# Kernel tuning notes

Hardware: AMD Instinct MI355X
Metric: run time of the kernel (lower is better)

The kernel has to match this reference:

```python
import jax, jax.numpy as jnp
import numpy as np

HEADS = 16
HEAD_DIM = 64
EMBED = HEADS * HEAD_DIM  # 1024
B, S = 2, 2048


def setup_inputs() -> dict:
    key = jax.random.key(0)
    ks = jax.random.split(key, 9)
    return {
        "value": jax.random.normal(ks[0], (B, S, EMBED), dtype=jnp.float32),
        "key": jax.random.normal(ks[1], (B, S, EMBED), dtype=jnp.float32),
        "query": jax.random.normal(ks[2], (B, S, EMBED), dtype=jnp.float32),
        "mask": jax.random.randint(ks[3], (B, 1, S, S), 0, 2, dtype=jnp.int32),
        "Wq": jax.random.normal(ks[4], (HEAD_DIM, HEAD_DIM), dtype=jnp.float32) * 0.02,
        "Wk": jax.random.normal(ks[5], (HEAD_DIM, HEAD_DIM), dtype=jnp.float32) * 0.02,
        "Wv": jax.random.normal(ks[6], (HEAD_DIM, HEAD_DIM), dtype=jnp.float32) * 0.02,
        "Wo": jax.random.normal(ks[7], (EMBED, EMBED), dtype=jnp.float32) * 0.02,
        "bo": jnp.zeros((EMBED,), dtype=jnp.float32),
    }


def reference(value, key, query, mask, Wq, Wk, Wv, Wo, bo):
    N, Lv = value.shape[0], value.shape[1]
    Lk, Lq = key.shape[1], query.shape[1]
    # Faithful to original: plain reshape (N, heads, len, head_dim), NOT transpose.
    v = value.reshape(N, HEADS, Lv, HEAD_DIM)
    k = key.reshape(N, HEADS, Lk, HEAD_DIM)
    q = query.reshape(N, HEADS, Lq, HEAD_DIM)
    # Per-head Linear (no bias): x @ W.T
    V = jnp.einsum('bhld,ed->bhle', v, Wv)
    K = jnp.einsum('bhld,ed->bhle', k, Wk)
    Q = jnp.einsum('bhld,ed->bhle', q, Wq)
    score = jnp.einsum('bhqd,bhkd->bhqk', Q, K)  # [B,H,Sq,Sk]
    score = jnp.where(mask == 0, jnp.float32(-1e20), score)
    # Faithful quirk: scale by sqrt(embed_size), not sqrt(head_dim)
    scale = jnp.float32(EMBED ** 0.5)
    attn = jax.nn.softmax(score / scale, axis=3)
    out = jnp.einsum('bhqk,bhkd->bhqd', attn, V).reshape(N, Lq, HEADS * HEAD_DIM)
    return out @ Wo.T + bo
```

## Files before the change

### kernel.cpp

```cpp
#include <hip/hip_runtime.h>
#include <hip/hip_bf16.h>
#include <cstdint>
#include <cstddef>

#define S_LEN 2048
#define N_HEADS 16
#define HD 64
#define EMB 1024
#define N_BATCH 2
#define N_BH (N_BATCH * N_HEADS)

typedef __attribute__((ext_vector_type(4))) float f32x4;
typedef __attribute__((ext_vector_type(8))) short bf16x8;
typedef __attribute__((ext_vector_type(4))) short bf16x4;

__device__ __forceinline__ short f2bf(float f) {
    unsigned u = __builtin_bit_cast(unsigned, f);
    unsigned r = (u + 0x7FFFu + ((u >> 16) & 1u)) >> 16;
    return (short)r;
}

__device__ __forceinline__ unsigned packbf(float a, float b) {
    return (unsigned)(unsigned short)f2bf(a) | ((unsigned)(unsigned short)f2bf(b) << 16);
}

__device__ __forceinline__ f32x4 mfma16(bf16x8 a, bf16x8 b, f32x4 c) {
    return __builtin_amdgcn_mfma_f32_16x16x32_bf16(a, b, c, 0, 0, 0);
}

#if __has_builtin(__builtin_amdgcn_exp2f)
__device__ __forceinline__ float fast_exp2(float x) { return __builtin_amdgcn_exp2f(x); }
#else
__device__ __forceinline__ float fast_exp2(float x) { return exp2f(x); }
#endif

__global__ __launch_bounds__(256) void pack_mask_kernel(
    const int* __restrict__ mask, unsigned long long* __restrict__ bits) {
    int wid = (blockIdx.x * 256 + threadIdx.x) >> 6;
    int lane = threadIdx.x & 63;
    const int* src = mask + (size_t)wid * 256 + lane;
    unsigned long long w0 = __ballot(src[0] != 0);
    unsigned long long w1 = __ballot(src[64] != 0);
    unsigned long long w2 = __ballot(src[128] != 0);
    unsigned long long w3 = __ballot(src[192] != 0);
    if (lane == 0) {
        unsigned long long* dst = bits + (size_t)wid * 4;
        dst[0] = w0; dst[1] = w1; dst[2] = w2; dst[3] = w3;
    }
}

__global__ __launch_bounds__(256) void conv_wo_kernel(
    const float* __restrict__ W, short* __restrict__ Wb) {
    int i = blockIdx.x * 256 + threadIdx.x;
    f32x4 v = reinterpret_cast<const f32x4*>(W)[i];
    bf16x4 o = { f2bf(v.x), f2bf(v.y), f2bf(v.z), f2bf(v.w) };
    reinterpret_cast<bf16x4*>(Wb)[i] = o;
}

__global__ __launch_bounds__(256) void proj_kernel(
    const float* __restrict__ q_in, const float* __restrict__ k_in,
    const float* __restrict__ v_in,
    const float* __restrict__ Wq, const float* __restrict__ Wk,
    const float* __restrict__ Wv,
    short* __restrict__ Qb, short* __restrict__ Kb, short* __restrict__ Vt) {
    int rt = blockIdx.x;
    int bh = blockIdx.y;
    int tz = blockIdx.z;
    const float* src = (tz == 0 ? q_in : tz == 1 ? k_in : v_in)
                       + (size_t)bh * S_LEN * HD + (size_t)rt * 64 * HD;
    const float* W = (tz == 0 ? Wq : tz == 1 ? Wk : Wv);

    __shared__ short Al[64 * 72];
    __shared__ short Wl[64 * 72];
    __shared__ short Ol[64 * 72];

    int t = threadIdx.x;
#pragma unroll
    for (int r = 0; r < 4; r++) {
        int f4 = t + 256 * r;
        int row = f4 >> 4;
        int c4 = (f4 & 15) * 4;
        f32x4 a = reinterpret_cast<const f32x4*>(src)[f4];
        bf16x4 ab = { f2bf(a.x), f2bf(a.y), f2bf(a.z), f2bf(a.w) };
        *reinterpret_cast<bf16x4*>(&Al[row * 72 + c4]) = ab;
        f32x4 w = reinterpret_cast<const f32x4*>(W)[f4];
        bf16x4 wb = { f2bf(w.x), f2bf(w.y), f2bf(w.z), f2bf(w.w) };
        *reinterpret_cast<bf16x4*>(&Wl[row * 72 + c4]) = wb;
    }
    __syncthreads();

    int wave = t >> 6, lane = t & 63, quad = lane >> 4, col = lane & 15;
    bf16x8 a0 = *reinterpret_cast<const bf16x8*>(&Al[(wave * 16 + col) * 72 + quad * 8]);
    bf16x8 a1 = *reinterpret_cast<const bf16x8*>(&Al[(wave * 16 + col) * 72 + 32 + quad * 8]);

    const float C1 = 0.04508422002777448f;
    float scl = (tz == 0) ? C1 : 1.0f;

    f32x4 acc[4];
#pragma unroll
    for (int jt = 0; jt < 4; jt++) {
        bf16x8 b0 = *reinterpret_cast<const bf16x8*>(&Wl[(jt * 16 + col) * 72 + quad * 8]);
        bf16x8 b1 = *reinterpret_cast<const bf16x8*>(&Wl[(jt * 16 + col) * 72 + 32 + quad * 8]);
        f32x4 c = {0.f, 0.f, 0.f, 0.f};
        c = mfma16(a0, b0, c);
        c = mfma16(a1, b1, c);
        acc[jt] = c;
    }
    __syncthreads();

    if (tz < 2) {
#pragma unroll
        for (int jt = 0; jt < 4; jt++)
#pragma unroll
            for (int i = 0; i < 4; i++)
                Ol[(wave * 16 + quad * 4 + i) * 72 + jt * 16 + col] = f2bf(acc[jt][i] * scl);
        __syncthreads();
        short* dst = (tz == 0 ? Qb : Kb) + (size_t)bh * S_LEN * HD + (size_t)rt * 64 * HD;
        int row = t >> 2, ck = (t & 3) * 16;
        bf16x8 o0 = *reinterpret_cast<const bf16x8*>(&Ol[row * 72 + ck]);
        bf16x8 o1 = *reinterpret_cast<const bf16x8*>(&Ol[row * 72 + ck + 8]);
        *reinterpret_cast<bf16x8*>(&dst[row * 64 + ck]) = o0;
        *reinterpret_cast<bf16x8*>(&dst[row * 64 + ck + 8]) = o1;
    } else {
#pragma unroll
        for (int jt = 0; jt < 4; jt++)
#pragma unroll
            for (int i = 0; i < 4; i++)
                Ol[(jt * 16 + col) * 72 + wave * 16 + quad * 4 + i] = f2bf(acc[jt][i]);
        __syncthreads();
        short* dst = Vt + (size_t)bh * HD * S_LEN + rt * 64;
        int d = t >> 2, ck = (t & 3) * 16;
        bf16x8 o0 = *reinterpret_cast<const bf16x8*>(&Ol[d * 72 + ck]);
        bf16x8 o1 = *reinterpret_cast<const bf16x8*>(&Ol[d * 72 + ck + 8]);
        *reinterpret_cast<bf16x8*>(&dst[(size_t)d * S_LEN + ck]) = o0;
        *reinterpret_cast<bf16x8*>(&dst[(size_t)d * S_LEN + ck + 8]) = o1;
    }
}

__global__ __launch_bounds__(256, 4) void attn_kernel(
    const short* __restrict__ Qb, const short* __restrict__ Kb,
    const short* __restrict__ Vt, const unsigned long long* __restrict__ mbits,
    short* __restrict__ Xb) {
    int qt = blockIdx.x;
    int bh = blockIdx.y;
    int b = bh >> 4;
    int t = threadIdx.x, wave = t >> 6, lane = t & 63, quad = lane >> 4, col = lane & 15;

    __shared__ short Ks[64 * 64];
    __shared__ short Vs[64 * 64];
    __shared__ short Pl[4][16 * 72];
    short* Pw = &Pl[wave][0];

    const short* Qh = Qb + (size_t)bh * S_LEN * HD;
    const short* Kh = Kb + (size_t)bh * S_LEN * HD;
    const short* Vh = Vt + (size_t)bh * HD * S_LEN;
    int q0w = qt * 64 + wave * 16;
    int q = q0w + col;

    bf16x8 qf0 = *reinterpret_cast<const bf16x8*>(&Qh[(size_t)q * HD + quad * 8]);
    bf16x8 qf1 = *reinterpret_cast<const bf16x8*>(&Qh[(size_t)q * HD + 32 + quad * 8]);
    const unsigned long long* mrow = mbits + (size_t)(b * S_LEN + q) * 32;

    int r0 = t >> 3, r1 = (t + 256) >> 3, cc = t & 7;
    int dst0 = r0 * 64 + ((cc ^ (r0 & 7)) * 8);
    int dst1 = r1 * 64 + ((cc ^ (r1 & 7)) * 8);
    const short* kg0 = Kh + r0 * HD + cc * 8;
    const short* kg1 = Kh + r1 * HD + cc * 8;
    const short* vg0 = Vh + (size_t)r0 * S_LEN + cc * 8;
    const short* vg1 = Vh + (size_t)r1 * S_LEN + cc * 8;

    bf16x8 pk0 = *reinterpret_cast<const bf16x8*>(kg0);
    bf16x8 pk1 = *reinterpret_cast<const bf16x8*>(kg1);
    bf16x8 pv0 = *reinterpret_cast<const bf16x8*>(vg0);
    bf16x8 pv1 = *reinterpret_cast<const bf16x8*>(vg1);
    *reinterpret_cast<bf16x8*>(&Ks[dst0]) = pk0;
    *reinterpret_cast<bf16x8*>(&Ks[dst1]) = pk1;
    *reinterpret_cast<bf16x8*>(&Vs[dst0]) = pv0;
    *reinterpret_cast<bf16x8*>(&Vs[dst1]) = pv1;
    __syncthreads();

    unsigned bs[4];
#pragma unroll
    for (int i = 0; i < 4; i++) bs[i] = 1u << (quad * 4 + i);
    const short one_bf = (short)0x3F80;
    bf16x8 ones = { one_bf, one_bf, one_bf, one_bf, one_bf, one_bf, one_bf, one_bf };

    int sw = quad ^ (col & 7);
    unsigned long long mw = mrow[0];

    f32x4 o[4];
    f32x4 l = {0.f, 0.f, 0.f, 0.f};
#pragma unroll
    for (int dt = 0; dt < 4; dt++) o[dt] = (f32x4){0.f, 0.f, 0.f, 0.f};

    for (int kt = 0; kt < 32; kt++) {
        unsigned long long mw_n;
        if (kt < 31) {
            pk0 = *reinterpret_cast<const bf16x8*>(kg0 + (kt + 1) * 4096);
            pk1 = *reinterpret_cast<const bf16x8*>(kg1 + (kt + 1) * 4096);
            pv0 = *reinterpret_cast<const bf16x8*>(vg0 + (kt + 1) * 64);
            pv1 = *reinterpret_cast<const bf16x8*>(vg1 + (kt + 1) * 64);
            mw_n = mrow[kt + 1];
        }
        f32x4 s[4];
#pragma unroll
        for (int mt = 0; mt < 4; mt++) {
            const short* kbase = &Ks[(mt * 16 + col) * 64];
            bf16x8 ka0 = *reinterpret_cast<const bf16x8*>(&kbase[sw * 8]);
            bf16x8 ka1 = *reinterpret_cast<const bf16x8*>(&kbase[(sw ^ 4) * 8]);
            f32x4 c = {0.f, 0.f, 0.f, 0.f};
            c = mfma16(ka0, qf0, c);
            c = mfma16(ka1, qf1, c);
            s[mt] = c;
        }
#pragma unroll
        for (int mt = 0; mt < 4; mt++) {
            unsigned g = (unsigned)(mw >> (mt * 16));
            float p0 = fast_exp2((g & bs[0]) ? s[mt][0] : -200.0f);
            float p1 = fast_exp2((g & bs[1]) ? s[mt][1] : -200.0f);
            float p2 = fast_exp2((g & bs[2]) ? s[mt][2] : -200.0f);
            float p3 = fast_exp2((g & bs[3]) ? s[mt][3] : -200.0f);
            uint2 dw = { packbf(p0, p1), packbf(p2, p3) };
            *reinterpret_cast<uint2*>(&Pw[col * 72 + mt * 16 + quad * 4]) = dw;
        }
#pragma unroll
        for (int c = 0; c < 2; c++) {
            bf16x8 pb = *reinterpret_cast<const bf16x8*>(&Pw[col * 72 + c * 32 + quad * 8]);
            l = mfma16(ones, pb, l);
#pragma unroll
            for (int dt = 0; dt < 4; dt++) {
                bf16x8 va = *reinterpret_cast<const bf16x8*>(
                    &Vs[(dt * 16 + col) * 64 + (((c * 4 + quad) ^ (col & 7)) * 8)]);
                o[dt] = mfma16(va, pb, o[dt]);
            }
        }
        __syncthreads();
        if (kt < 31) {
            *reinterpret_cast<bf16x8*>(&Ks[dst0]) = pk0;
            *reinterpret_cast<bf16x8*>(&Ks[dst1]) = pk1;
            *reinterpret_cast<bf16x8*>(&Vs[dst0]) = pv0;
            *reinterpret_cast<bf16x8*>(&Vs[dst1]) = pv1;
            mw = mw_n;
            __syncthreads();
        }
    }

    float inv = 1.0f / l[0];
#pragma unroll
    for (int dt = 0; dt < 4; dt++) {
        uint2 dw = { packbf(o[dt][0] * inv, o[dt][1] * inv),
                     packbf(o[dt][2] * inv, o[dt][3] * inv) };
        *reinterpret_cast<uint2*>(&Pw[col * 72 + dt * 16 + quad * 4]) = dw;
    }
    int rr = lane >> 2, ck = (lane & 3) * 16;
    bf16x8 x0 = *reinterpret_cast<const bf16x8*>(&Pw[rr * 72 + ck]);
    bf16x8 x1 = *reinterpret_cast<const bf16x8*>(&Pw[rr * 72 + ck + 8]);
    short* Xrow = Xb + (size_t)bh * S_LEN * HD + (size_t)(q0w + rr) * HD;
    *reinterpret_cast<bf16x8*>(&Xrow[ck]) = x0;
    *reinterpret_cast<bf16x8*>(&Xrow[ck + 8]) = x1;
}

__global__ __launch_bounds__(256, 4) void final_kernel(
    const short* __restrict__ Xb, const short* __restrict__ Wob,
    const float* __restrict__ bo, float* __restrict__ out) {
    int nb = blockIdx.x;
    int mb = blockIdx.y;
    int t = threadIdx.x, wave = t >> 6, lane = t & 63, quad = lane >> 4, col = lane & 15;
    __shared__ short Xs[64 * 64];
    __shared__ short Ws[64 * 64];
    __shared__ float Olds[64 * 68];

    int m0 = mb * 64, n0 = nb * 64;
    int r0 = t >> 3, r1 = (t + 256) >> 3, cc = t & 7;
    int dst0 = r0 * 64 + ((cc ^ (r0 & 7)) * 8);
    int dst1 = r1 * 64 + ((cc ^ (r1 & 7)) * 8);
    const short* xg0 = Xb + (size_t)(m0 + r0) * EMB + cc * 8;
    const short* xg1 = Xb + (size_t)(m0 + r1) * EMB + cc * 8;
    const short* wg0 = Wob + (size_t)(n0 + r0) * EMB + cc * 8;
    const short* wg1 = Wob + (size_t)(n0 + r1) * EMB + cc * 8;

    bf16x8 px0 = *reinterpret_cast<const bf16x8*>(xg0);
    bf16x8 px1 = *reinterpret_cast<const bf16x8*>(xg1);
    bf16x8 pw0 = *reinterpret_cast<const bf16x8*>(wg0);
    bf16x8 pw1 = *reinterpret_cast<const bf16x8*>(wg1);
    *reinterpret_cast<bf16x8*>(&Xs[dst0]) = px0;
    *reinterpret_cast<bf16x8*>(&Xs[dst1]) = px1;
    *reinterpret_cast<bf16x8*>(&Ws[dst0]) = pw0;
    *reinterpret_cast<bf16x8*>(&Ws[dst1]) = pw1;
    __syncthreads();

    int sw = quad ^ (col & 7);
    f32x4 acc[4];
#pragma unroll
    for (int jt = 0; jt < 4; jt++) acc[jt] = (f32x4){0.f, 0.f, 0.f, 0.f};

    for (int s = 0; s < 16; s++) {
        if (s < 15) {
            px0 = *reinterpret_cast<const bf16x8*>(xg0 + (s + 1) * 64);
            px1 = *reinterpret_cast<const bf16x8*>(xg1 + (s + 1) * 64);
            pw0 = *reinterpret_cast<const bf16x8*>(wg0 + (s + 1) * 64);
            pw1 = *reinterpret_cast<const bf16x8*>(wg1 + (s + 1) * 64);
        }
        const short* arow = &Xs[(wave * 16 + col) * 64];
        bf16x8 a0 = *reinterpret_cast<const bf16x8*>(&arow[sw * 8]);
        bf16x8 a1 = *reinterpret_cast<const bf16x8*>(&arow[(sw ^ 4) * 8]);
#pragma unroll
        for (int jt = 0; jt < 4; jt++) {
            const short* brow = &Ws[(jt * 16 + col) * 64];
            bf16x8 b0 = *reinterpret_cast<const bf16x8*>(&brow[sw * 8]);
            bf16x8 b1 = *reinterpret_cast<const bf16x8*>(&brow[(sw ^ 4) * 8]);
            acc[jt] = mfma16(a0, b0, acc[jt]);
            acc[jt] = mfma16(a1, b1, acc[jt]);
        }
        __syncthreads();
        if (s < 15) {
            *reinterpret_cast<bf16x8*>(&Xs[dst0]) = px0;
            *reinterpret_cast<bf16x8*>(&Xs[dst1]) = px1;
            *reinterpret_cast<bf16x8*>(&Ws[dst0]) = pw0;
            *reinterpret_cast<bf16x8*>(&Ws[dst1]) = pw1;
            __syncthreads();
        }
    }

#pragma unroll
    for (int jt = 0; jt < 4; jt++)
#pragma unroll
        for (int i = 0; i < 4; i++)
            Olds[(wave * 16 + quad * 4 + i) * 68 + jt * 16 + col] = acc[jt][i];
    __syncthreads();
    int row = t >> 2, ck = (t & 3) * 16;
#pragma unroll
    for (int u = 0; u < 4; u++) {
        f32x4 v = *reinterpret_cast<const f32x4*>(&Olds[row * 68 + ck + u * 4]);
        f32x4 bb = *reinterpret_cast<const f32x4*>(&bo[n0 + ck + u * 4]);
        v.x += bb.x; v.y += bb.y; v.z += bb.z; v.w += bb.w;
        *reinterpret_cast<f32x4*>(&out[(size_t)(m0 + row) * EMB + n0 + ck + u * 4]) = v;
    }
}

extern "C" void kernel_launch(void* const* d_in, const int* in_sizes, int n_in,
                              void* d_out, int out_size, void* d_ws, size_t ws_size,
                              hipStream_t stream) {
    const float* value = (const float*)d_in[0];
    const float* key_  = (const float*)d_in[1];
    const float* query = (const float*)d_in[2];
    const int*   mask  = (const int*)d_in[3];
    const float* Wq = (const float*)d_in[4];
    const float* Wk = (const float*)d_in[5];
    const float* Wv = (const float*)d_in[6];
    const float* Wo = (const float*)d_in[7];
    const float* bo = (const float*)d_in[8];
    float* out = (float*)d_out;

    char* ws = (char*)d_ws;
    short* Qb  = (short*)(ws);
    short* Kb  = (short*)(ws + (size_t)8  * 1048576);
    short* Vt  = (short*)(ws + (size_t)16 * 1048576);
    short* Xb  = (short*)(ws + (size_t)24 * 1048576);
    short* Wob = (short*)(ws + (size_t)32 * 1048576);
    unsigned long long* mbits =
        (unsigned long long*)(ws + (size_t)34 * 1048576);

    pack_mask_kernel<<<dim3((N_BATCH * S_LEN * S_LEN) / 1024), dim3(256), 0, stream>>>(mask, mbits);
    conv_wo_kernel<<<dim3((EMB * EMB) / (256 * 4)), dim3(256), 0, stream>>>(Wo, Wob);
    proj_kernel<<<dim3(S_LEN / 64, N_BH, 3), dim3(256), 0, stream>>>(
        query, key_, value, Wq, Wk, Wv, Qb, Kb, Vt);
    attn_kernel<<<dim3(S_LEN / 64, N_BH), dim3(256), 0, stream>>>(Qb, Kb, Vt, mbits, Xb);
    final_kernel<<<dim3(EMB / 64, (N_BATCH * S_LEN) / 64), dim3(256), 0, stream>>>(
        Xb, Wob, bo, out);
}
```

Before: 217.6 us.

## Switch to fp16 MFMA, merge prep kernels, use 128-query attention blocks

Merges mask packing, Wo conversion and the Q/K/V projections into one prep launch, removing two kernel launches. Replaces bf16 with fp16 throughout, using packed round-toward-zero conversion and fp16 MFMA, which cuts the conversion instruction count. Attention blocks now use 512 threads covering 128 queries, so each K/V tile staged in shared memory serves twice as many queries and each thread loads half as much. fp16 range is a risk for unnormalized values, but the inputs here appear scaled small.

```diff
diff --git a/kernel.cpp b/kernel.cpp
--- a/kernel.cpp
+++ b/kernel.cpp
@@ -11,21 +11,16 @@
 #define N_BH (N_BATCH * N_HEADS)
 
 typedef __attribute__((ext_vector_type(4))) float f32x4;
-typedef __attribute__((ext_vector_type(8))) short bf16x8;
-typedef __attribute__((ext_vector_type(4))) short bf16x4;
-
-__device__ __forceinline__ short f2bf(float f) {
-    unsigned u = __builtin_bit_cast(unsigned, f);
-    unsigned r = (u + 0x7FFFu + ((u >> 16) & 1u)) >> 16;
-    return (short)r;
-}
-
-__device__ __forceinline__ unsigned packbf(float a, float b) {
-    return (unsigned)(unsigned short)f2bf(a) | ((unsigned)(unsigned short)f2bf(b) << 16);
-}
-
-__device__ __forceinline__ f32x4 mfma16(bf16x8 a, bf16x8 b, f32x4 c) {
-    return __builtin_amdgcn_mfma_f32_16x16x32_bf16(a, b, c, 0, 0, 0);
+typedef __attribute__((ext_vector_type(8))) short short8;
+typedef __attribute__((ext_vector_type(8))) _Float16 half8;
+typedef __attribute__((ext_vector_type(2))) _Float16 half2v;
+
+__device__ __forceinline__ f32x4 mfma16h(half8 a, half8 b, f32x4 c) {
+    return __builtin_amdgcn_mfma_f32_16x16x32_f16(a, b, c, 0, 0, 0);
+}
+
+__device__ __forceinline__ unsigned pkh(float a, float b) {
+    return __builtin_bit_cast(unsigned, __builtin_amdgcn_cvt_pkrtz(a, b));
 }
 
 #if __has_builtin(__builtin_amdgcn_exp2f)
@@ -34,64 +29,67 @@
 __device__ __forceinline__ float fast_exp2(float x) { return exp2f(x); }
 #endif
 
-__global__ __launch_bounds__(256) void pack_mask_kernel(
-    const int* __restrict__ mask, unsigned long long* __restrict__ bits) {
-    int wid = (blockIdx.x * 256 + threadIdx.x) >> 6;
-    int lane = threadIdx.x & 63;
-    const int* src = mask + (size_t)wid * 256 + lane;
-    unsigned long long w0 = __ballot(src[0] != 0);
-    unsigned long long w1 = __ballot(src[64] != 0);
-    unsigned long long w2 = __ballot(src[128] != 0);
-    unsigned long long w3 = __ballot(src[192] != 0);
-    if (lane == 0) {
-        unsigned long long* dst = bits + (size_t)wid * 4;
-        dst[0] = w0; dst[1] = w1; dst[2] = w2; dst[3] = w3;
-    }
-}
-
-__global__ __launch_bounds__(256) void conv_wo_kernel(
-    const float* __restrict__ W, short* __restrict__ Wb) {
-    int i = blockIdx.x * 256 + threadIdx.x;
-    f32x4 v = reinterpret_cast<const f32x4*>(W)[i];
-    bf16x4 o = { f2bf(v.x), f2bf(v.y), f2bf(v.z), f2bf(v.w) };
-    reinterpret_cast<bf16x4*>(Wb)[i] = o;
-}
-
-__global__ __launch_bounds__(256) void proj_kernel(
+__global__ __launch_bounds__(256) void prep_kernel(
     const float* __restrict__ q_in, const float* __restrict__ k_in,
     const float* __restrict__ v_in,
     const float* __restrict__ Wq, const float* __restrict__ Wk,
-    const float* __restrict__ Wv,
-    short* __restrict__ Qb, short* __restrict__ Kb, short* __restrict__ Vt) {
-    int rt = blockIdx.x;
-    int bh = blockIdx.y;
-    int tz = blockIdx.z;
+    const float* __restrict__ Wv, const float* __restrict__ Wo,
+    const int* __restrict__ mask,
+    short* __restrict__ Qb, short* __restrict__ Kb, short* __restrict__ Vt,
+    short* __restrict__ Woh, unsigned long long* __restrict__ bits) {
+    __shared__ short Al[64 * 72];
+    __shared__ short Wl[64 * 72];
+    __shared__ short Ol[64 * 72];
+    int bx = blockIdx.x;
+    int t = threadIdx.x;
+
+    if (bx >= 3072) {
+        if (bx < 11264) {
+            int wid = ((bx - 3072) * 256 + t) >> 6;
+            int lane = t & 63;
+            const int* src = mask + (size_t)wid * 256 + lane;
+            unsigned long long w0 = __ballot(src[0] != 0);
+            unsigned long long w1 = __ballot(src[64] != 0);
+            unsigned long long w2 = __ballot(src[128] != 0);
+            unsigned long long w3 = __ballot(src[192] != 0);
+            if (lane == 0) {
+                unsigned long long* dst = bits + (size_t)wid * 4;
+                dst[0] = w0; dst[1] = w1; dst[2] = w2; dst[3] = w3;
+            }
+        } else {
+            int i = (bx - 11264) * 256 + t;
+            f32x4 a = reinterpret_cast<const f32x4*>(Wo)[i * 2];
+            f32x4 b = reinterpret_cast<const f32x4*>(Wo)[i * 2 + 1];
+            uint4 u = { pkh(a.x, a.y), pkh(a.z, a.w), pkh(b.x, b.y), pkh(b.z, b.w) };
+            reinterpret_cast<uint4*>(Woh)[i] = u;
+        }
+        return;
+    }
+
+    int rt = bx & 31;
+    int bh = (bx >> 5) & 31;
+    int tz = bx >> 10;
     const float* src = (tz == 0 ? q_in : tz == 1 ? k_in : v_in)
                        + (size_t)bh * S_LEN * HD + (size_t)rt * 64 * HD;
     const float* W = (tz == 0 ? Wq : tz == 1 ? Wk : Wv);
 
-    __shared__ short Al[64 * 72];
-    __shared__ short Wl[64 * 72];
-    __shared__ short Ol[64 * 72];
-
-    int t = threadIdx.x;
 #pragma unroll
     for (int r = 0; r < 4; r++) {
         int f4 = t + 256 * r;
         int row = f4 >> 4;
         int c4 = (f4 & 15) * 4;
         f32x4 a = reinterpret_cast<const f32x4*>(src)[f4];
-        bf16x4 ab = { f2bf(a.x), f2bf(a.y), f2bf(a.z), f2bf(a.w) };
-        *reinterpret_cast<bf16x4*>(&Al[row * 72 + c4]) = ab;
+        uint2 ua = { pkh(a.x, a.y), pkh(a.z, a.w) };
+        *reinterpret_cast<uint2*>(&Al[row * 72 + c4]) = ua;
         f32x4 w = reinterpret_cast<const f32x4*>(W)[f4];
-        bf16x4 wb = { f2bf(w.x), f2bf(w.y), f2bf(w.z), f2bf(w.w) };
-        *reinterpret_cast<bf16x4*>(&Wl[row * 72 + c4]) = wb;
+        uint2 uw = { pkh(w.x, w.y), pkh(w.z, w.w) };
+        *reinterpret_cast<uint2*>(&Wl[row * 72 + c4]) = uw;
     }
     __syncthreads();
 
     int wave = t >> 6, lane = t & 63, quad = lane >> 4, col = lane & 15;
-    bf16x8 a0 = *reinterpret_cast<const bf16x8*>(&Al[(wave * 16 + col) * 72 + quad * 8]);
-    bf16x8 a1 = *reinterpret_cast<const bf16x8*>(&Al[(wave * 16 + col) * 72 + 32 + quad * 8]);
+    half8 a0 = *reinterpret_cast<const half8*>(&Al[(wave * 16 + col) * 72 + quad * 8]);
+    half8 a1 = *reinterpret_cast<const half8*>(&Al[(wave * 16 + col) * 72 + 32 + quad * 8]);
 
     const float C1 = 0.04508422002777448f;
     float scl = (tz == 0) ? C1 : 1.0f;
@@ -99,11 +97,11 @@
     f32x4 acc[4];
 #pragma unroll
     for (int jt = 0; jt < 4; jt++) {
-        bf16x8 b0 = *reinterpret_cast<const bf16x8*>(&Wl[(jt * 16 + col) * 72 + quad * 8]);
-        bf16x8 b1 = *reinterpret_cast<const bf16x8*>(&Wl[(jt * 16 + col) * 72 + 32 + quad * 8]);
+        half8 b0 = *reinterpret_cast<const half8*>(&Wl[(jt * 16 + col) * 72 + quad * 8]);
+        half8 b1 = *reinterpret_cast<const half8*>(&Wl[(jt * 16 + col) * 72 + 32 + quad * 8]);
         f32x4 c = {0.f, 0.f, 0.f, 0.f};
-        c = mfma16(a0, b0, c);
-        c = mfma16(a1, b1, c);
+        c = mfma16h(a0, b0, c);
+        c = mfma16h(a1, b1, c);
         acc[jt] = c;
     }
     __syncthreads();
@@ -113,31 +111,33 @@
         for (int jt = 0; jt < 4; jt++)
 #pragma unroll
             for (int i = 0; i < 4; i++)
-                Ol[(wave * 16 + quad * 4 + i) * 72 + jt * 16 + col] = f2bf(acc[jt][i] * scl);
+                Ol[(wave * 16 + quad * 4 + i) * 72 + jt * 16 + col] =
+                    __builtin_bit_cast(short, (_Float16)(acc[jt][i] * scl));
         __syncthreads();
         short* dst = (tz == 0 ? Qb : Kb) + (size_t)bh * S_LEN * HD + (size_t)rt * 64 * HD;
         int row = t >> 2, ck = (t & 3) * 16;
-        bf16x8 o0 = *reinterpret_cast<const bf16x8*>(&Ol[row * 72 + ck]);
-        bf16x8 o1 = *reinterpret_cast<const bf16x8*>(&Ol[row * 72 + ck + 8]);
-        *reinterpret_cast<bf16x8*>(&dst[row * 64 + ck]) = o0;
-        *reinterpret_cast<bf16x8*>(&dst[row * 64 + ck + 8]) = o1;
+        short8 o0 = *reinterpret_cast<const short8*>(&Ol[row * 72 + ck]);
+        short8 o1 = *reinterpret_cast<const short8*>(&Ol[row * 72 + ck + 8]);
+        *reinterpret_cast<short8*>(&dst[row * 64 + ck]) = o0;
+        *reinterpret_cast<short8*>(&dst[row * 64 + ck + 8]) = o1;
     } else {
 #pragma unroll
         for (int jt = 0; jt < 4; jt++)
 #pragma unroll
             for (int i = 0; i < 4; i++)
-                Ol[(jt * 16 + col) * 72 + wave * 16 + quad * 4 + i] = f2bf(acc[jt][i]);
+                Ol[(jt * 16 + col) * 72 + wave * 16 + quad * 4 + i] =
+                    __builtin_bit_cast(short, (_Float16)acc[jt][i]);
         __syncthreads();
         short* dst = Vt + (size_t)bh * HD * S_LEN + rt * 64;
         int d = t >> 2, ck = (t & 3) * 16;
-        bf16x8 o0 = *reinterpret_cast<const bf16x8*>(&Ol[d * 72 + ck]);
-        bf16x8 o1 = *reinterpret_cast<const bf16x8*>(&Ol[d * 72 + ck + 8]);
-        *reinterpret_cast<bf16x8*>(&dst[(size_t)d * S_LEN + ck]) = o0;
-        *reinterpret_cast<bf16x8*>(&dst[(size_t)d * S_LEN + ck + 8]) = o1;
-    }
-}
-
-__global__ __launch_bounds__(256, 4) void attn_kernel(
+        short8 o0 = *reinterpret_cast<const short8*>(&Ol[d * 72 + ck]);
+        short8 o1 = *reinterpret_cast<const short8*>(&Ol[d * 72 + ck + 8]);
+        *reinterpret_cast<short8*>(&dst[(size_t)d * S_LEN + ck]) = o0;
+        *reinterpret_cast<short8*>(&dst[(size_t)d * S_LEN + ck + 8]) = o1;
+    }
+}
+
+__global__ __launch_bounds__(512, 4) void attn_kernel(
     const short* __restrict__ Qb, const short* __restrict__ Kb,
     const short* __restrict__ Vt, const unsigned long long* __restrict__ mbits,
     short* __restrict__ Xb) {
@@ -148,42 +148,35 @@
 
     __shared__ short Ks[64 * 64];
     __shared__ short Vs[64 * 64];
-    __shared__ short Pl[4][16 * 72];
+    __shared__ short Pl[8][16 * 72];
     short* Pw = &Pl[wave][0];
 
     const short* Qh = Qb + (size_t)bh * S_LEN * HD;
     const short* Kh = Kb + (size_t)bh * S_LEN * HD;
     const short* Vh = Vt + (size_t)bh * HD * S_LEN;
-    int q0w = qt * 64 + wave * 16;
+    int q0w = qt * 128 + wave * 16;
     int q = q0w + col;
 
-    bf16x8 qf0 = *reinterpret_cast<const bf16x8*>(&Qh[(size_t)q * HD + quad * 8]);
-    bf16x8 qf1 = *reinterpret_cast<const bf16x8*>(&Qh[(size_t)q * HD + 32 + quad * 8]);
+    half8 qf0 = *reinterpret_cast<const half8*>(&Qh[(size_t)q * HD + quad * 8]);
+    half8 qf1 = *reinterpret_cast<const half8*>(&Qh[(size_t)q * HD + 32 + quad * 8]);
     const unsigned long long* mrow = mbits + (size_t)(b * S_LEN + q) * 32;
 
-    int r0 = t >> 3, r1 = (t + 256) >> 3, cc = t & 7;
+    int r0 = t >> 3, cc = t & 7;
     int dst0 = r0 * 64 + ((cc ^ (r0 & 7)) * 8);
-    int dst1 = r1 * 64 + ((cc ^ (r1 & 7)) * 8);
     const short* kg0 = Kh + r0 * HD + cc * 8;
-    const short* kg1 = Kh + r1 * HD + cc * 8;
     const short* vg0 = Vh + (size_t)r0 * S_LEN + cc * 8;
-    const short* vg1 = Vh + (size_t)r1 * S_LEN + cc * 8;
-
-    bf16x8 pk0 = *reinterpret_cast<const bf16x8*>(kg0);
-    bf16x8 pk1 = *reinterpret_cast<const bf16x8*>(kg1);
-    bf16x8 pv0 = *reinterpret_cast<const bf16x8*>(vg0);
-    bf16x8 pv1 = *reinterpret_cast<const bf16x8*>(vg1);
-    *reinterpret_cast<bf16x8*>(&Ks[dst0]) = pk0;
-    *reinterpret_cast<bf16x8*>(&Ks[dst1]) = pk1;
-    *reinterpret_cast<bf16x8*>(&Vs[dst0]) = pv0;
-    *reinterpret_cast<bf16x8*>(&Vs[dst1]) = pv1;
+
+    short8 pk0 = *reinterpret_cast<const short8*>(kg0);
+    short8 pv0 = *reinterpret_cast<const short8*>(vg0);
+    *reinterpret_cast<short8*>(&Ks[dst0]) = pk0;
+    *reinterpret_cast<short8*>(&Vs[dst0]) = pv0;
     __syncthreads();
 
     unsigned bs[4];
 #pragma unroll
     for (int i = 0; i < 4; i++) bs[i] = 1u << (quad * 4 + i);
-    const short one_bf = (short)0x3F80;
-    bf16x8 ones = { one_bf, one_bf, one_bf, one_bf, one_bf, one_bf, one_bf, one_bf };
+    half8 ones = { (_Float16)1.f, (_Float16)1.f, (_Float16)1.f, (_Float16)1.f,
+                   (_Float16)1.f, (_Float16)1.f, (_Float16)1.f, (_Float16)1.f };
 
     int sw = quad ^ (col & 7);
     unsigned long long mw = mrow[0];
@@ -196,21 +189,19 @@
     for (int kt = 0; kt < 32; kt++) {
         unsigned long long mw_n;
         if (kt < 31) {
-            pk0 = *reinterpret_cast<const bf16x8*>(kg0 + (kt + 1) * 4096);
-            pk1 = *reinterpret_cast<const bf16x8*>(kg1 + (kt + 1) * 4096);
-            pv0 = *reinterpret_cast<const bf16x8*>(vg0 + (kt + 1) * 64);
-            pv1 = *reinterpret_cast<const bf16x8*>(vg1 + (kt + 1) * 64);
+            pk0 = *reinterpret_cast<const short8*>(kg0 + (kt + 1) * 4096);
+            pv0 = *reinterpret_cast<const short8*>(vg0 + (kt + 1) * 64);
             mw_n = mrow[kt + 1];
         }
         f32x4 s[4];
 #pragma unroll
         for (int mt = 0; mt < 4; mt++) {
             const short* kbase = &Ks[(mt * 16 + col) * 64];
-            bf16x8 ka0 = *reinterpret_cast<const bf16x8*>(&kbase[sw * 8]);
-            bf16x8 ka1 = *reinterpret_cast<const bf16x8*>(&kbase[(sw ^ 4) * 8]);
+            half8 ka0 = *reinterpret_cast<const half8*>(&kbase[sw * 8]);
+            half8 ka1 = *reinterpret_cast<const half8*>(&kbase[(sw ^ 4) * 8]);
             f32x4 c = {0.f, 0.f, 0.f, 0.f};
-            c = mfma16(ka0, qf0, c);
-            c = mfma16(ka1, qf1, c);
+            c = mfma16h(ka0, qf0, c);
+            c = mfma16h(ka1, qf1, c);
             s[mt] = c;
         }
 #pragma unroll
@@ -220,26 +211,24 @@
             float p1 = fast_exp2((g & bs[1]) ? s[mt][1] : -200.0f);
             float p2 = fast_exp2((g & bs[2]) ? s[mt][2] : -200.0f);
             float p3 = fast_exp2((g & bs[3]) ? s[mt][3] : -200.0f);
-            uint2 dw = { packbf(p0, p1), packbf(p2, p3) };
+            uint2 dw = { pkh(p0, p1), pkh(p2, p3) };
             *reinterpret_cast<uint2*>(&Pw[col * 72 + mt * 16 + quad * 4]) = dw;
         }
 #pragma unroll
         for (int c = 0; c < 2; c++) {
-            bf16x8 pb = *reinterpret_cast<const bf16x8*>(&Pw[col * 72 + c * 32 + quad * 8]);
-            l = mfma16(ones, pb, l);
+            half8 pb = *reinterpret_cast<const half8*>(&Pw[col * 72 + c * 32 + quad * 8]);
+            l = mfma16h(ones, pb, l);
 #pragma unroll
             for (int dt = 0; dt < 4; dt++) {
-                bf16x8 va = *reinterpret_cast<const bf16x8*>(
+                half8 va = *reinterpret_cast<const half8*>(
                     &Vs[(dt * 16 + col) * 64 + (((c * 4 + quad) ^ (col & 7)) * 8)]);
-                o[dt] = mfma16(va, pb, o[dt]);
+                o[dt] = mfma16h(va, pb, o[dt]);
             }
         }
         __syncthreads();
         if (kt < 31) {
-            *reinterpret_cast<bf16x8*>(&Ks[dst0]) = pk0;
-            *reinterpret_cast<bf16x8*>(&Ks[dst1]) = pk1;
-            *reinterpret_cast<bf16x8*>(&Vs[dst0]) = pv0;
-            *reinterpret_cast<bf16x8*>(&Vs[dst1]) = pv1;
+            *reinterpret_cast<short8*>(&Ks[dst0]) = pk0;
+            *reinterpret_cast<short8*>(&Vs[dst0]) = pv0;
             mw = mw_n;
             __syncthreads();
         }
@@ -248,20 +237,20 @@
     float inv = 1.0f / l[0];
 #pragma unroll
     for (int dt = 0; dt < 4; dt++) {
-        uint2 dw = { packbf(o[dt][0] * inv, o[dt][1] * inv),
-                     packbf(o[dt][2] * inv, o[dt][3] * inv) };
+        uint2 dw = { pkh(o[dt][0] * inv, o[dt][1] * inv),
+                     pkh(o[dt][2] * inv, o[dt][3] * inv) };
         *reinterpret_cast<uint2*>(&Pw[col * 72 + dt * 16 + quad * 4]) = dw;
     }
     int rr = lane >> 2, ck = (lane & 3) * 16;
-    bf16x8 x0 = *reinterpret_cast<const bf16x8*>(&Pw[rr * 72 + ck]);
-    bf16x8 x1 = *reinterpret_cast<const bf16x8*>(&Pw[rr * 72 + ck + 8]);
+    short8 x0 = *reinterpret_cast<const short8*>(&Pw[rr * 72 + ck]);
+    short8 x1 = *reinterpret_cast<const short8*>(&Pw[rr * 72 + ck + 8]);
     short* Xrow = Xb + (size_t)bh * S_LEN * HD + (size_t)(q0w + rr) * HD;
-    *reinterpret_cast<bf16x8*>(&Xrow[ck]) = x0;
-    *reinterpret_cast<bf16x8*>(&Xrow[ck + 8]) = x1;
+    *reinterpret_cast<short8*>(&Xrow[ck]) = x0;
+    *reinterpret_cast<short8*>(&Xrow[ck + 8]) = x1;
 }
 
 __global__ __launch_bounds__(256, 4) void final_kernel(
-    const short* __restrict__ Xb, const short* __restrict__ Wob,
+    const short* __restrict__ Xb, const short* __restrict__ Woh,
     const float* __restrict__ bo, float* __restrict__ out) {
     int nb = blockIdx.x;
     int mb = blockIdx.y;
@@ -276,17 +265,17 @@
     int dst1 = r1 * 64 + ((cc ^ (r1 & 7)) * 8);
     const short* xg0 = Xb + (size_t)(m0 + r0) * EMB + cc * 8;
     const short* xg1 = Xb + (size_t)(m0 + r1) * EMB + cc * 8;
-    const short* wg0 = Wob + (size_t)(n0 + r0) * EMB + cc * 8;
-    const short* wg1 = Wob + (size_t)(n0 + r1) * EMB + cc * 8;
-
-    bf16x8 px0 = *reinterpret_cast<const bf16x8*>(xg0);
-    bf16x8 px1 = *reinterpret_cast<const bf16x8*>(xg1);
-    bf16x8 pw0 = *reinterpret_cast<const bf16x8*>(wg0);
-    bf16x8 pw1 = *reinterpret_cast<const bf16x8*>(wg1);
-    *reinterpret_cast<bf16x8*>(&Xs[dst0]) = px0;
-    *reinterpret_cast<bf16x8*>(&Xs[dst1]) = px1;
-    *reinterpret_cast<bf16x8*>(&Ws[dst0]) = pw0;
-    *reinterpret_cast<bf16x8*>(&Ws[dst1]) = pw1;
+    const short* wg0 = Woh + (size_t)(n0 + r0) * EMB + cc * 8;
+    const short* wg1 = Woh + (size_t)(n0 + r1) * EMB + cc * 8;
+
+    short8 px0 = *reinterpret_cast<const short8*>(xg0);
+    short8 px1 = *reinterpret_cast<const short8*>(xg1);
+    short8 pw0 = *reinterpret_cast<const short8*>(wg0);
+    short8 pw1 = *reinterpret_cast<const short8*>(wg1);
+    *reinterpret_cast<short8*>(&Xs[dst0]) = px0;
+    *reinterpret_cast<short8*>(&Xs[dst1]) = px1;
+    *reinterpret_cast<short8*>(&Ws[dst0]) = pw0;
+    *reinterpret_cast<short8*>(&Ws[dst1]) = pw1;
     __syncthreads();
 
     int sw = quad ^ (col & 7);
@@ -296,28 +285,28 @@
 
     for (int s = 0; s < 16; s++) {
         if (s < 15) {
-            px0 = *reinterpret_cast<const bf16x8*>(xg0 + (s + 1) * 64);
-            px1 = *reinterpret_cast<const bf16x8*>(xg1 + (s + 1) * 64);
-            pw0 = *reinterpret_cast<const bf16x8*>(wg0 + (s + 1) * 64);
-            pw1 = *reinterpret_cast<const bf16x8*>(wg1 + (s + 1) * 64);
+            px0 = *reinterpret_cast<const short8*>(xg0 + (s + 1) * 64);
+            px1 = *reinterpret_cast<const short8*>(xg1 + (s + 1) * 64);
+            pw0 = *reinterpret_cast<const short8*>(wg0 + (s + 1) * 64);
+            pw1 = *reinterpret_cast<const short8*>(wg1 + (s + 1) * 64);
         }
         const short* arow = &Xs[(wave * 16 + col) * 64];
-        bf16x8 a0 = *reinterpret_cast<const bf16x8*>(&arow[sw * 8]);
-        bf16x8 a1 = *reinterpret_cast<const bf16x8*>(&arow[(sw ^ 4) * 8]);
+        half8 a0 = *reinterpret_cast<const half8*>(&arow[sw * 8]);
+        half8 a1 = *reinterpret_cast<const half8*>(&arow[(sw ^ 4) * 8]);
 #pragma unroll
         for (int jt = 0; jt < 4; jt++) {
             const short* brow = &Ws[(jt * 16 + col) * 64];
-            bf16x8 b0 = *reinterpret_cast<const bf16x8*>(&brow[sw * 8]);
-            bf16x8 b1 = *reinterpret_cast<const bf16x8*>(&brow[(sw ^ 4) * 8]);
-            acc[jt] = mfma16(a0, b0, acc[jt]);
-            acc[jt] = mfma16(a1, b1, acc[jt]);
+            half8 b0 = *reinterpret_cast<const half8*>(&brow[sw * 8]);
+            half8 b1 = *reinterpret_cast<const half8*>(&brow[(sw ^ 4) * 8]);
+            acc[jt] = mfma16h(a0, b0, acc[jt]);
+            acc[jt] = mfma16h(a1, b1, acc[jt]);
         }
         __syncthreads();
         if (s < 15) {
-            *reinterpret_cast<bf16x8*>(&Xs[dst0]) = px0;
-            *reinterpret_cast<bf16x8*>(&Xs[dst1]) = px1;
-            *reinterpret_cast<bf16x8*>(&Ws[dst0]) = pw0;
-            *reinterpret_cast<bf16x8*>(&Ws[dst1]) = pw1;
+            *reinterpret_cast<short8*>(&Xs[dst0]) = px0;
+            *reinterpret_cast<short8*>(&Xs[dst1]) = px1;
+            *reinterpret_cast<short8*>(&Ws[dst0]) = pw0;
+            *reinterpret_cast<short8*>(&Ws[dst1]) = pw1;
             __syncthreads();
         }
     }
@@ -357,15 +346,13 @@
     short* Kb  = (short*)(ws + (size_t)8  * 1048576);
     short* Vt  = (short*)(ws + (size_t)16 * 1048576);
     short* Xb  = (short*)(ws + (size_t)24 * 1048576);
-    short* Wob = (short*)(ws + (size_t)32 * 1048576);
+    short* Woh = (short*)(ws + (size_t)32 * 1048576);
     unsigned long long* mbits =
         (unsigned long long*)(ws + (size_t)34 * 1048576);
 
-    pack_mask_kernel<<<dim3((N_BATCH * S_LEN * S_LEN) / 1024), dim3(256), 0, stream>>>(mask, mbits);
-    conv_wo_kernel<<<dim3((EMB * EMB) / (256 * 4)), dim3(256), 0, stream>>>(Wo, Wob);
-    proj_kernel<<<dim3(S_LEN / 64, N_BH, 3), dim3(256), 0, stream>>>(
-        query, key_, value, Wq, Wk, Wv, Qb, Kb, Vt);
-    attn_kernel<<<dim3(S_LEN / 64, N_BH), dim3(256), 0, stream>>>(Qb, Kb, Vt, mbits, Xb);
+    prep_kernel<<<dim3(3072 + 8192 + 512), dim3(256), 0, stream>>>(
+        query, key_, value, Wq, Wk, Wv, Wo, mask, Qb, Kb, Vt, Woh, mbits);
+    attn_kernel<<<dim3(S_LEN / 128, N_BH), dim3(512), 0, stream>>>(Qb, Kb, Vt, mbits, Xb);
     final_kernel<<<dim3(EMB / 64, (N_BATCH * S_LEN) / 64), dim3(256), 0, stream>>>(
-        Xb, Wob, bo, out);
-}
+        Xb, Woh, bo, out);
+}
```

Result: faster. 204.7 us (-5.9%).
